# Kernel tuning notes

Measured on AMD Instinct MI355X. Metric: run time of the kernel, lower is better.

The kernel has to match this reference:

```python
import jax, jax.numpy as jnp
import numpy as np

B, N, H, F = 4, 512, 4096, 11008   # batch, seq, hidden, intermediate
L, R, RANK = 1, 16, 16             # layers stored, num adapters, lora rank
SCALE = 0.5                        # lora_scale


def setup_inputs() -> dict:
    key = jax.random.key(0)
    ks = jax.random.split(key, 12)
    nrm = lambda k, shape, fan: (jax.random.normal(k, shape, jnp.float32) * (fan ** -0.5))
    inp = {
        "x": jax.random.normal(ks[0], (B, N, H), jnp.float32),
        "W_gate": nrm(ks[1], (F, H), H),
        "W_up": nrm(ks[2], (F, H), H),
        "W_down": nrm(ks[3], (H, F), F),
        # LoRA tables: [num_layers, num_adapters, rank, in] and [num_layers, num_adapters, out, rank]
        "A_gate": nrm(ks[4], (L, R, RANK, H), H),
        "B_gate": nrm(ks[5], (L, R, F, RANK), RANK),
        "A_up": nrm(ks[6], (L, R, RANK, H), H),
        "B_up": nrm(ks[7], (L, R, F, RANK), RANK),
        "A_down": nrm(ks[8], (L, R, RANK, F), F),
        "B_down": nrm(ks[9], (L, R, H, RANK), RANK),
        "lora_indices": jax.random.randint(ks[10], (B,), 0, R),
        "layer_idx": 0,
    }
    return inp


def reference(x, W_gate, W_up, W_down, A_gate, B_gate, A_up, B_up,
              A_down, B_down, lora_indices, layer_idx):
    def lora_add(base, inp, A, B):
        # gather per-sequence adapter slices, then rank-r batched matmuls
        Ab = A[layer_idx][lora_indices]  # [B, r, in]
        Bb = B[layer_idx][lora_indices]  # [B, out, r]
        t = jnp.einsum('bri,bni->bnr', Ab, inp)        # down-project to rank
        return base + jnp.einsum('bor,bnr->bno', Bb, t) * SCALE

    gate = lora_add(jnp.einsum('bnh,fh->bnf', x, W_gate), x, A_gate, B_gate)
    up = lora_add(jnp.einsum('bnh,fh->bnf', x, W_up), x, A_up, B_up)
    act = jax.nn.silu(gate) * up                        # SwiGLU
    down = lora_add(jnp.einsum('bnf,hf->bnh', act, W_down), act, A_down, B_down)
    return down
```

## Files before the change

### kernel.cpp

```cpp
#include <hip/hip_runtime.h>
#include <hip/hip_bf16.h>

typedef __bf16 bf16x8 __attribute__((ext_vector_type(8)));
typedef float  f32x4  __attribute__((ext_vector_type(4)));
typedef unsigned short u16;

#define GLDS16(gsrc, ldst)                                                        \
  __builtin_amdgcn_global_load_lds(                                               \
      (const __attribute__((address_space(1))) unsigned int*)(gsrc),              \
      (__attribute__((address_space(3))) unsigned int*)(ldst), 16, 0, 0)

#define BAR() __builtin_amdgcn_s_barrier()
#define WAIT_LGKM0() asm volatile("s_waitcnt lgkmcnt(0)" ::: "memory")
#define WAIT_VM4() asm volatile("s_waitcnt vmcnt(4)" ::: "memory")

__device__ __forceinline__ u16 f2b(float f) {
  unsigned int u = __builtin_bit_cast(unsigned int, f);
  u = (u + 0x7fffu + ((u >> 16) & 1u)) >> 16;
  return (u16)u;
}
__device__ __forceinline__ float b2f(u16 b) {
  unsigned int u = ((unsigned int)b) << 16;
  return __builtin_bit_cast(float, u);
}

__global__ __launch_bounds__(256) void cvt3_kernel(
    const float4* __restrict__ xf,  ushort4* __restrict__ xb,
    const float4* __restrict__ wgf, ushort4* __restrict__ wgb,
    const float4* __restrict__ wuf, ushort4* __restrict__ wub) {
  const float4* in; ushort4* out; int i, stride, n4;
  if (blockIdx.x < 512) {
    in = xf; out = xb; n4 = 2097152;
    i = blockIdx.x * 256 + threadIdx.x; stride = 512 * 256;
  } else if (blockIdx.x < 2560) {
    in = wgf; out = wgb; n4 = 11272192;
    i = (blockIdx.x - 512) * 256 + threadIdx.x; stride = 2048 * 256;
  } else {
    in = wuf; out = wub; n4 = 11272192;
    i = (blockIdx.x - 2560) * 256 + threadIdx.x; stride = 2048 * 256;
  }
  for (; i < n4; i += stride) {
    float4 v = in[i];
    ushort4 o;
    o.x = f2b(v.x); o.y = f2b(v.y); o.z = f2b(v.z); o.w = f2b(v.w);
    out[i] = o;
  }
}

__global__ __launch_bounds__(256) void lora_t2(const u16* __restrict__ Xb, int K,
                                               const float* __restrict__ A1,
                                               const float* __restrict__ A2,
                                               const int* __restrict__ lidx,
                                               const int* __restrict__ layer,
                                               u16* __restrict__ t1,
                                               u16* __restrict__ t2) {
  __shared__ float red1[4][64][4];
  __shared__ float red2[4][64][4];
  const int lane = threadIdx.x & 63, wid = threadIdx.x >> 6;
  const int m0 = blockIdx.x * 16;
  const int li = lidx[m0 >> 9];
  const size_t abase = ((size_t)layer[0] * 16 + li) * 16 * (size_t)K;
  const int r = lane & 15, kg = lane >> 4;
  const int Kq = K >> 2, kb = wid * Kq;
  f32x4 acc1 = {0.f, 0.f, 0.f, 0.f}, acc2 = {0.f, 0.f, 0.f, 0.f};
  for (int k0 = kb; k0 < kb + Kq; k0 += 32) {
    bf16x8 a = *(const bf16x8*)&Xb[(size_t)(m0 + r) * K + k0 + kg * 8];
    const float* ap = A1 + abase + (size_t)r * K + k0 + kg * 8;
    float4 f0 = *(const float4*)ap;
    float4 f1 = *(const float4*)(ap + 4);
    bf16x8 b;
    b[0] = (__bf16)f0.x; b[1] = (__bf16)f0.y; b[2] = (__bf16)f0.z; b[3] = (__bf16)f0.w;
    b[4] = (__bf16)f1.x; b[5] = (__bf16)f1.y; b[6] = (__bf16)f1.z; b[7] = (__bf16)f1.w;
    acc1 = __builtin_amdgcn_mfma_f32_16x16x32_bf16(a, b, acc1, 0, 0, 0);
    if (A2) {
      const float* ap2 = A2 + abase + (size_t)r * K + k0 + kg * 8;
      float4 g0 = *(const float4*)ap2;
      float4 g1 = *(const float4*)(ap2 + 4);
      bf16x8 b2;
      b2[0] = (__bf16)g0.x; b2[1] = (__bf16)g0.y; b2[2] = (__bf16)g0.z; b2[3] = (__bf16)g0.w;
      b2[4] = (__bf16)g1.x; b2[5] = (__bf16)g1.y; b2[6] = (__bf16)g1.z; b2[7] = (__bf16)g1.w;
      acc2 = __builtin_amdgcn_mfma_f32_16x16x32_bf16(a, b2, acc2, 0, 0, 0);
    }
  }
#pragma unroll
  for (int j = 0; j < 4; ++j) {
    red1[wid][lane][j] = acc1[j];
    if (A2) red2[wid][lane][j] = acc2[j];
  }
  __syncthreads();
  if (wid == 0) {
#pragma unroll
    for (int j = 0; j < 4; ++j) {
      int m = m0 + kg * 4 + j;
      float v1 = red1[0][lane][j] + red1[1][lane][j] + red1[2][lane][j] + red1[3][lane][j];
      t1[(size_t)m * 16 + r] = f2b(0.5f * v1);
      if (A2) {
        float v2 = red2[0][lane][j] + red2[1][lane][j] + red2[2][lane][j] + red2[3][lane][j];
        t2[(size_t)m * 16 + r] = f2b(0.5f * v2);
      }
    }
  }
}

#define RD_A(dst, buf, mh) do {                                                \
    _Pragma("unroll")                                                          \
    for (int mf_ = 0; mf_ < 4; ++mf_)                                          \
      _Pragma("unroll")                                                        \
      for (int ks_ = 0; ks_ < 2; ++ks_) {                                      \
        int row_ = wm * 128 + (mh) * 64 + mf_ * 16 + lr;                       \
        int sl_ = (ks_ * 4 + kg) ^ rx;                                         \
        dst[mf_][ks_] = *(const bf16x8*)&sA[(buf) * 16384 + row_ * 64 + sl_ * 8]; \
      }                                                                        \
  } while (0)

#define RD_B(dst, buf, nh) do {                                                \
    _Pragma("unroll")                                                          \
    for (int nf_ = 0; nf_ < 2; ++nf_)                                          \
      _Pragma("unroll")                                                        \
      for (int ks_ = 0; ks_ < 2; ++ks_) {                                      \
        int row_ = wn * 64 + (nh) * 32 + nf_ * 16 + lr;                        \
        int sl_ = (ks_ * 4 + kg) ^ rx;                                         \
        dst[nf_][ks_] = *(const bf16x8*)&sB[(buf) * 16384 + row_ * 64 + sl_ * 8]; \
      }                                                                        \
  } while (0)

#define RD_BW(dst, SB, buf) do {                                               \
    _Pragma("unroll")                                                          \
    for (int nf_ = 0; nf_ < 2; ++nf_)                                          \
      _Pragma("unroll")                                                        \
      for (int ks_ = 0; ks_ < 2; ++ks_) {                                      \
        int row_ = wn * 32 + nf_ * 16 + lr;                                    \
        int sl_ = (ks_ * 4 + kg) ^ rx;                                         \
        dst[nf_][ks_] = *(const bf16x8*)&SB[(buf) * 8192 + row_ * 64 + sl_ * 8]; \
      }                                                                        \
  } while (0)

#define MMA_Q(AF, BF, mb, nb) do {                                             \
    __builtin_amdgcn_s_setprio(1);                                             \
    _Pragma("unroll")                                                          \
    for (int mf_ = 0; mf_ < 4; ++mf_)                                          \
      _Pragma("unroll")                                                        \
      for (int nf_ = 0; nf_ < 2; ++nf_)                                        \
        _Pragma("unroll")                                                      \
        for (int ks_ = 0; ks_ < 2; ++ks_)                                      \
          acc[(mb) + mf_][(nb) + nf_] = __builtin_amdgcn_mfma_f32_16x16x32_bf16( \
              AF[mf_][ks_], BF[nf_][ks_], acc[(mb) + mf_][(nb) + nf_], 0, 0, 0); \
    __builtin_amdgcn_s_setprio(0);                                             \
  } while (0)

#define MMA_F(AF, BF, ACC, mb) do {                                            \
    __builtin_amdgcn_s_setprio(1);                                             \
    _Pragma("unroll")                                                          \
    for (int mf_ = 0; mf_ < 4; ++mf_)                                          \
      _Pragma("unroll")                                                        \
      for (int nf_ = 0; nf_ < 2; ++nf_)                                        \
        _Pragma("unroll")                                                      \
        for (int ks_ = 0; ks_ < 2; ++ks_)                                      \
          ACC[(mb) + mf_][nf_] = __builtin_amdgcn_mfma_f32_16x16x32_bf16(      \
              AF[mf_][ks_], BF[nf_][ks_], ACC[(mb) + mf_][nf_], 0, 0, 0);      \
    __builtin_amdgcn_s_setprio(0);                                             \
  } while (0)

#define STAGE_F(buf, half, kt) do {                                            \
    const u16* gs_; u16* ld_;                                                  \
    if ((half) == 0)      { gs_ = Xb + (size_t)m0 * 4096 + (size_t)(kt) * 64;         ld_ = sA  + (buf) * 16384; }        \
    else if ((half) == 1) { gs_ = Xb + (size_t)(m0 + 128) * 4096 + (size_t)(kt) * 64; ld_ = sA  + (buf) * 16384 + 8192; } \
    else if ((half) == 2) { gs_ = Wg + (size_t)n0 * 4096 + (size_t)(kt) * 64;         ld_ = sBG + (buf) * 8192; }         \
    else                  { gs_ = Wu + (size_t)n0 * 4096 + (size_t)(kt) * 64;         ld_ = sBU + (buf) * 8192; }         \
    _Pragma("unroll")                                                          \
    for (int i_ = 0; i_ < 2; ++i_) {                                           \
      int ub_ = (wid << 6) + i_ * 512;                                         \
      int un_ = ub_ + lane;                                                    \
      int ur_ = un_ >> 3, us_ = (un_ & 7) ^ (ur_ & 7);                         \
      GLDS16(gs_ + (size_t)ur_ * 4096 + us_ * 8, ld_ + ub_ * 8);               \
    }                                                                          \
  } while (0)

__global__ __launch_bounds__(512, 2) void gemm_gup_fused(
    const u16* __restrict__ Xb, const u16* __restrict__ Wg, const u16* __restrict__ Wu,
    const u16* __restrict__ tg, const u16* __restrict__ tu,
    const float* __restrict__ Bg, const float* __restrict__ Bu,
    const int* __restrict__ lidx, const int* __restrict__ layer,
    u16* __restrict__ act,
    const float4* __restrict__ Wdf, ushort4* __restrict__ wdb3) {
  constexpr int F = 11008;
  const int b = blockIdx.x;
  if (b >= 704) {
    int i = (b - 704) * 512 + threadIdx.x;
    for (; i < 11272192; i += 256 * 512) {
      float4 v = Wdf[i];
      ushort4 o;
      o.x = f2b(v.x); o.y = f2b(v.y); o.z = f2b(v.z); o.w = f2b(v.w);
      wdb3[i] = o;
    }
    return;
  }
  const int xcd = b & 7, j = b >> 3;
  const int ny = xcd + 8 * (j >> 3);
  const int mx = j & 7;
  if (ny >= 86) return;
  extern __shared__ u16 smem[];
  u16* sA  = smem;
  u16* sBG = smem + 32768;
  u16* sBU = smem + 49152;
  const int tid = threadIdx.x, lane = tid & 63, wid = tid >> 6;
  const int lr = lane & 15, kg = lane >> 4, rx = lr & 7;
  const int wm = wid >> 2, wn = wid & 3;
  const int m0 = mx * 256;
  const int n0 = ny * 128;

  f32x4 accg[8][2] = {}, accu[8][2] = {};
  bf16x8 a0[4][2], a1[4][2], bg[2][2], bu[2][2];

  STAGE_F(0, 0, 0); STAGE_F(0, 1, 0); STAGE_F(0, 2, 0); STAGE_F(0, 3, 0);
  STAGE_F(1, 2, 1); STAGE_F(1, 3, 1);
  WAIT_VM4(); BAR();

#pragma unroll 1
  for (int u = 0; u < 32; ++u) {
    const int ktA = (2 * u + 1) & 63;
    const int kt0 = (2 * u + 2) & 63;
    const int kt1 = (2 * u + 3) & 63;
    RD_A(a0, 0, 0); RD_BW(bg, sBG, 0);
    STAGE_F(1, 0, ktA);
    BAR(); WAIT_LGKM0();
    MMA_F(a0, bg, accg, 0);
    BAR();
    RD_BW(bu, sBU, 0);
    STAGE_F(1, 1, ktA);
    BAR(); WAIT_LGKM0();
    MMA_F(a0, bu, accu, 0);
    BAR();
    RD_A(a1, 0, 1);
    STAGE_F(0, 2, kt0);
    BAR(); WAIT_LGKM0();
    MMA_F(a1, bu, accu, 4);
    BAR();
    STAGE_F(0, 3, kt0);
    BAR();
    MMA_F(a1, bg, accg, 4);
    WAIT_VM4();
    BAR();
    RD_A(a0, 1, 0); RD_BW(bg, sBG, 1);
    STAGE_F(0, 0, kt0); STAGE_F(0, 1, kt0);
    BAR(); WAIT_LGKM0();
    MMA_F(a0, bg, accg, 0);
    BAR();
    RD_BW(bu, sBU, 1);
    BAR(); WAIT_LGKM0();
    MMA_F(a0, bu, accu, 0);
    BAR();
    RD_A(a1, 1, 1);
    STAGE_F(1, 2, kt1);
    BAR(); WAIT_LGKM0();
    MMA_F(a1, bu, accu, 4);
    BAR();
    STAGE_F(1, 3, kt1);
    BAR();
    MMA_F(a1, bg, accg, 4);
    WAIT_VM4();
    BAR();
  }

  const int li = lidx[m0 >> 9];
  const size_t bbase = ((size_t)layer[0] * 16 + li) * (size_t)F * 16;
  bf16x8 la[8], lb[2];
  const bf16x8 zz = {};
#pragma unroll
  for (int mf = 0; mf < 8; ++mf) {
    int row = m0 + wm * 128 + mf * 16 + lr;
    la[mf] = (kg < 2) ? *(const bf16x8*)&tg[(size_t)row * 16 + kg * 8] : zz;
  }
#pragma unroll
  for (int nf = 0; nf < 2; ++nf) {
    int col = n0 + wn * 32 + nf * 16 + lr;
    if (kg < 2) {
      const float* bp = Bg + bbase + (size_t)col * 16 + kg * 8;
      float4 f0 = *(const float4*)bp;
      float4 f1 = *(const float4*)(bp + 4);
      bf16x8 v;
      v[0] = (__bf16)f0.x; v[1] = (__bf16)f0.y; v[2] = (__bf16)f0.z; v[3] = (__bf16)f0.w;
      v[4] = (__bf16)f1.x; v[5] = (__bf16)f1.y; v[6] = (__bf16)f1.z; v[7] = (__bf16)f1.w;
      lb[nf] = v;
    } else lb[nf] = zz;
  }
#pragma unroll
  for (int mf = 0; mf < 8; ++mf)
#pragma unroll
    for (int nf = 0; nf < 2; ++nf)
      accg[mf][nf] = __builtin_amdgcn_mfma_f32_16x16x32_bf16(la[mf], lb[nf], accg[mf][nf], 0, 0, 0);
#pragma unroll
  for (int mf = 0; mf < 8; ++mf) {
    int row = m0 + wm * 128 + mf * 16 + lr;
    la[mf] = (kg < 2) ? *(const bf16x8*)&tu[(size_t)row * 16 + kg * 8] : zz;
  }
#pragma unroll
  for (int nf = 0; nf < 2; ++nf) {
    int col = n0 + wn * 32 + nf * 16 + lr;
    if (kg < 2) {
      const float* bp = Bu + bbase + (size_t)col * 16 + kg * 8;
      float4 f0 = *(const float4*)bp;
      float4 f1 = *(const float4*)(bp + 4);
      bf16x8 v;
      v[0] = (__bf16)f0.x; v[1] = (__bf16)f0.y; v[2] = (__bf16)f0.z; v[3] = (__bf16)f0.w;
      v[4] = (__bf16)f1.x; v[5] = (__bf16)f1.y; v[6] = (__bf16)f1.z; v[7] = (__bf16)f1.w;
      lb[nf] = v;
    } else lb[nf] = zz;
  }
#pragma unroll
  for (int mf = 0; mf < 8; ++mf)
#pragma unroll
    for (int nf = 0; nf < 2; ++nf)
      accu[mf][nf] = __builtin_amdgcn_mfma_f32_16x16x32_bf16(la[mf], lb[nf], accu[mf][nf], 0, 0, 0);

#pragma unroll
  for (int mf = 0; mf < 8; ++mf)
#pragma unroll
    for (int nf = 0; nf < 2; ++nf)
#pragma unroll
      for (int j2 = 0; j2 < 4; ++j2) {
        int row = m0 + wm * 128 + mf * 16 + kg * 4 + j2;
        int col = n0 + wn * 32 + nf * 16 + lr;
        float g = accg[mf][nf][j2], uu = accu[mf][nf][j2];
        float s = g / (1.f + __expf(-g));
        act[(size_t)row * F + col] = f2b(s * uu);
      }
}

#define STAGE_D(buf, half, kt) do {                                           \
    int r0_ = ((half) & 1) * 128;                                             \
    const u16* gs_ = ((half) < 2)                                             \
        ? (Ab + (size_t)(m0 + r0_) * 11008 + (size_t)(kt) * 64)               \
        : (Wd + (size_t)(n0 + r0_) * 11008 + (size_t)(kt) * 64);              \
    u16* ld_ = (((half) < 2) ? sA : sB) + (buf) * 16384 + r0_ * 64;           \
    _Pragma("unroll")                                                         \
    for (int i_ = 0; i_ < 2; ++i_) {                                          \
      int ub_ = (wid << 6) + i_ * 512;                                        \
      int un_ = ub_ + lane;                                                   \
      int ur_ = un_ >> 3, us_ = (un_ & 7) ^ (ur_ & 7);                        \
      GLDS16(gs_ + (size_t)ur_ * 11008 + us_ * 8, ld_ + ub_ * 8);             \
    }                                                                         \
  } while (0)

#define KT(t) (kbase + ((t) >= 86 ? (t) - 86 : (t)))

__global__ __launch_bounds__(512, 2) void gemm_down8(
    const u16* __restrict__ Ab, const u16* __restrict__ Wd,
    const u16* __restrict__ td, const float* __restrict__ Bd,
    const int* __restrict__ lidx, const int* __restrict__ layer,
    float* __restrict__ P0, float* __restrict__ P1) {
  constexpr int H = 4096;
  extern __shared__ u16 smem[];
  u16* sA = smem;
  u16* sB = smem + 32768;
  const int tid = threadIdx.x, lane = tid & 63, wid = tid >> 6;
  const int lr = lane & 15, kg = lane >> 4, rx = lr & 7;
  const int wm = wid >> 2, wn = wid & 3;
  const int m0 = blockIdx.x * 256, n0 = blockIdx.y * 256;
  const int kbase = blockIdx.z * 86;
  float* P = blockIdx.z ? P1 : P0;

  f32x4 acc[8][4] = {};
  bf16x8 a0[4][2], a1[4][2], b0[2][2], b1[2][2];

  STAGE_D(0, 0, KT(0)); STAGE_D(0, 1, KT(0)); STAGE_D(0, 2, KT(0)); STAGE_D(0, 3, KT(0));
  STAGE_D(1, 2, KT(1)); STAGE_D(1, 3, KT(1));
  WAIT_VM4(); BAR();

#pragma unroll 1
  for (int u = 0; u < 43; ++u) {
    const int ktA = KT(2 * u + 1);
    const int kt0 = KT(2 * u + 2);
    const int kt1 = KT(2 * u + 3);
    RD_A(a0, 0, 0); RD_B(b0, 0, 0);
    STAGE_D(1, 0, ktA);
    BAR(); WAIT_LGKM0();
    MMA_Q(a0, b0, 0, 0);
    BAR();
    RD_B(b1, 0, 1);
    STAGE_D(1, 1, ktA);
    BAR(); WAIT_LGKM0();
    MMA_Q(a0, b1, 0, 2);
    BAR();
    RD_A(a1, 0, 1);
    STAGE_D(0, 2, kt0);
    BAR(); WAIT_LGKM0();
    MMA_Q(a1, b1, 4, 2);
    BAR();
    STAGE_D(0, 3, kt0);
    BAR();
    MMA_Q(a1, b0, 4, 0);
    WAIT_VM4();
    BAR();
    RD_A(a0, 1, 0); RD_B(b0, 1, 0);
    STAGE_D(0, 0, kt0);
    BAR(); WAIT_LGKM0();
    MMA_Q(a0, b0, 0, 0);
    BAR();
    RD_B(b1, 1, 1);
    STAGE_D(0, 1, kt0);
    BAR(); WAIT_LGKM0();
    MMA_Q(a0, b1, 0, 2);
    BAR();
    RD_A(a1, 1, 1);
    STAGE_D(1, 2, kt1);
    BAR(); WAIT_LGKM0();
    MMA_Q(a1, b1, 4, 2);
    BAR();
    STAGE_D(1, 3, kt1);
    BAR();
    MMA_Q(a1, b0, 4, 0);
    WAIT_VM4();
    BAR();
  }

  if (blockIdx.z == 0) {
    const int li = lidx[m0 >> 9];
    const size_t bbase = ((size_t)layer[0] * 16 + li) * (size_t)H * 16;
    bf16x8 la[8], lb[4];
    const bf16x8 zz = {};
#pragma unroll
    for (int mf = 0; mf < 8; ++mf) {
      int row = m0 + wm * 128 + mf * 16 + lr;
      la[mf] = (kg < 2) ? *(const bf16x8*)&td[(size_t)row * 16 + kg * 8] : zz;
    }
#pragma unroll
    for (int nf = 0; nf < 4; ++nf) {
      int col = n0 + wn * 64 + nf * 16 + lr;
      if (kg < 2) {
        const float* bp = Bd + bbase + (size_t)col * 16 + kg * 8;
        float4 f0 = *(const float4*)bp;
        float4 f1 = *(const float4*)(bp + 4);
        bf16x8 v;
        v[0] = (__bf16)f0.x; v[1] = (__bf16)f0.y; v[2] = (__bf16)f0.z; v[3] = (__bf16)f0.w;
        v[4] = (__bf16)f1.x; v[5] = (__bf16)f1.y; v[6] = (__bf16)f1.z; v[7] = (__bf16)f1.w;
        lb[nf] = v;
      } else lb[nf] = zz;
    }
#pragma unroll
    for (int mf = 0; mf < 8; ++mf)
#pragma unroll
      for (int nf = 0; nf < 4; ++nf)
        acc[mf][nf] = __builtin_amdgcn_mfma_f32_16x16x32_bf16(la[mf], lb[nf], acc[mf][nf], 0, 0, 0);
  }

#pragma unroll
  for (int mf = 0; mf < 8; ++mf)
#pragma unroll
    for (int nf = 0; nf < 4; ++nf)
#pragma unroll
      for (int j = 0; j < 4; ++j) {
        int row = m0 + wm * 128 + mf * 16 + kg * 4 + j;
        int col = n0 + wn * 64 + nf * 16 + lr;
        P[(size_t)row * H + col] = acc[mf][nf][j];
      }
}

__global__ __launch_bounds__(256) void combine_down(
    const float4* __restrict__ P0, const float4* __restrict__ P1,
    float4* __restrict__ out) {
  int gid = blockIdx.x * 256 + threadIdx.x;
  float4 p0 = P0[gid], p1 = P1[gid];
  out[gid] = make_float4(p0.x + p1.x, p0.y + p1.y, p0.z + p1.z, p0.w + p1.w);
}

extern "C" void kernel_launch(void* const* d_in, const int* in_sizes, int n_in,
                              void* d_out, int out_size, void* d_ws, size_t ws_size,
                              hipStream_t stream) {
  const float* x  = (const float*)d_in[0];
  const float* Wg = (const float*)d_in[1];
  const float* Wu = (const float*)d_in[2];
  const float* Wd = (const float*)d_in[3];
  const float* Ag = (const float*)d_in[4];
  const float* Bg = (const float*)d_in[5];
  const float* Au = (const float*)d_in[6];
  const float* Bu = (const float*)d_in[7];
  const float* Ad = (const float*)d_in[8];
  const float* Bd = (const float*)d_in[9];
  const int* lidx = (const int*)d_in[10];
  const int* lay  = (const int*)d_in[11];
  float* out = (float*)d_out;

  char* ws = (char*)d_ws;
  u16*  xb   = (u16*)(ws + 0);
  u16*  wgb  = (u16*)(ws + 16777216);
  u16*  wub  = (u16*)(ws + 106954752);
  u16*  gbuf = (u16*)(ws + 197132288);
  u16*  tg   = (u16*)(ws + 287309824);
  u16*  tu   = (u16*)(ws + 287375360);
  u16*  td   = (u16*)(ws + 287440896);
  u16*  wdb3 = (u16*)(ws + 287506432);
  float* P0  = (float*)(ws + 242221056);
  float* P1  = (float*)wub;

  hipFuncSetAttribute(reinterpret_cast<const void*>(gemm_gup_fused),
                      hipFuncAttributeMaxDynamicSharedMemorySize, 131072);
  hipFuncSetAttribute(reinterpret_cast<const void*>(gemm_down8),
                      hipFuncAttributeMaxDynamicSharedMemorySize, 131072);

  cvt3_kernel<<<4608, 256, 0, stream>>>((const float4*)x,  (ushort4*)xb,
                                        (const float4*)Wg, (ushort4*)wgb,
                                        (const float4*)Wu, (ushort4*)wub);

  lora_t2<<<128, 256, 0, stream>>>(xb, 4096, Ag, Au, lidx, lay, tg, tu);

  gemm_gup_fused<<<dim3(960), 512, 131072, stream>>>(
      xb, wgb, wub, tg, tu, Bg, Bu, lidx, lay, gbuf,
      (const float4*)Wd, (ushort4*)wdb3);

  lora_t2<<<128, 256, 0, stream>>>(gbuf, 11008, Ad, nullptr, lidx, lay, td, nullptr);

  gemm_down8<<<dim3(8, 16, 2), 512, 131072, stream>>>(gbuf, wdb3, td, Bd, lidx, lay,
                                                      P0, P1);

  combine_down<<<8192, 256, 0, stream>>>((const float4*)P0, (const float4*)P1,
                                         (float4*)out);
}
```

Measured before the change: 732.8 us.

## Replace split-K down GEMM and combine pass with 256x128 tiles writing output directly

The down-projection GEMM previously used 256x256 tiles with a 2-way K split, writing two fp32 partial buffers that a separate combine kernel summed. The new kernel uses 256x128 tiles over the full K range, 256 blocks mapped by an XCD-aware index, and writes the final output directly with the LoRA term added. This removes the partial-buffer writes and reads and one kernel launch. In exchange, each block reads more A data per unit of work, runs a longer K loop, and uses a different staging schedule with less shared memory.

```diff
diff --git a/kernel.cpp b/kernel.cpp
--- a/kernel.cpp
+++ b/kernel.cpp
@@ -12,6 +12,7 @@
 
 #define BAR() __builtin_amdgcn_s_barrier()
 #define WAIT_LGKM0() asm volatile("s_waitcnt lgkmcnt(0)" ::: "memory")
+#define WAIT_VM0() asm volatile("s_waitcnt vmcnt(0)" ::: "memory")
 #define WAIT_VM4() asm volatile("s_waitcnt vmcnt(4)" ::: "memory")
 
 __device__ __forceinline__ u16 f2b(float f) {
@@ -113,17 +114,6 @@
       }                                                                        \
   } while (0)
 
-#define RD_B(dst, buf, nh) do {                                                \
-    _Pragma("unroll")                                                          \
-    for (int nf_ = 0; nf_ < 2; ++nf_)                                          \
-      _Pragma("unroll")                                                        \
-      for (int ks_ = 0; ks_ < 2; ++ks_) {                                      \
-        int row_ = wn * 64 + (nh) * 32 + nf_ * 16 + lr;                        \
-        int sl_ = (ks_ * 4 + kg) ^ rx;                                         \
-        dst[nf_][ks_] = *(const bf16x8*)&sB[(buf) * 16384 + row_ * 64 + sl_ * 8]; \
-      }                                                                        \
-  } while (0)
-
 #define RD_BW(dst, SB, buf) do {                                               \
     _Pragma("unroll")                                                          \
     for (int nf_ = 0; nf_ < 2; ++nf_)                                          \
@@ -133,19 +123,6 @@
         int sl_ = (ks_ * 4 + kg) ^ rx;                                         \
         dst[nf_][ks_] = *(const bf16x8*)&SB[(buf) * 8192 + row_ * 64 + sl_ * 8]; \
       }                                                                        \
-  } while (0)
-
-#define MMA_Q(AF, BF, mb, nb) do {                                             \
-    __builtin_amdgcn_s_setprio(1);                                             \
-    _Pragma("unroll")                                                          \
-    for (int mf_ = 0; mf_ < 4; ++mf_)                                          \
-      _Pragma("unroll")                                                        \
-      for (int nf_ = 0; nf_ < 2; ++nf_)                                        \
-        _Pragma("unroll")                                                      \
-        for (int ks_ = 0; ks_ < 2; ++ks_)                                      \
-          acc[(mb) + mf_][(nb) + nf_] = __builtin_amdgcn_mfma_f32_16x16x32_bf16( \
-              AF[mf_][ks_], BF[nf_][ks_], acc[(mb) + mf_][(nb) + nf_], 0, 0, 0); \
-    __builtin_amdgcn_s_setprio(0);                                             \
   } while (0)
 
 #define MMA_F(AF, BF, ACC, mb) do {                                            \
@@ -327,141 +304,125 @@
       }
 }
 
-#define STAGE_D(buf, half, kt) do {                                           \
-    int r0_ = ((half) & 1) * 128;                                             \
-    const u16* gs_ = ((half) < 2)                                             \
-        ? (Ab + (size_t)(m0 + r0_) * 11008 + (size_t)(kt) * 64)               \
-        : (Wd + (size_t)(n0 + r0_) * 11008 + (size_t)(kt) * 64);              \
-    u16* ld_ = (((half) < 2) ? sA : sB) + (buf) * 16384 + r0_ * 64;           \
-    _Pragma("unroll")                                                         \
-    for (int i_ = 0; i_ < 2; ++i_) {                                          \
-      int ub_ = (wid << 6) + i_ * 512;                                        \
-      int un_ = ub_ + lane;                                                   \
-      int ur_ = un_ >> 3, us_ = (un_ & 7) ^ (ur_ & 7);                        \
-      GLDS16(gs_ + (size_t)ur_ * 11008 + us_ * 8, ld_ + ub_ * 8);             \
-    }                                                                         \
-  } while (0)
-
-#define KT(t) (kbase + ((t) >= 86 ? (t) - 86 : (t)))
-
-__global__ __launch_bounds__(512, 2) void gemm_down8(
+#define STAGE_NA(buf, half, kt) do {                                           \
+    const u16* gs_ = Ab + (size_t)(m0 + (half) * 128) * 11008 + (size_t)(kt) * 64; \
+    u16* ld_ = sA + (buf) * 16384 + (half) * 8192;                             \
+    _Pragma("unroll")                                                          \
+    for (int i_ = 0; i_ < 2; ++i_) {                                           \
+      int ub_ = (wid << 6) + i_ * 512;                                         \
+      int un_ = ub_ + lane;                                                    \
+      int ur_ = un_ >> 3, us_ = (un_ & 7) ^ (ur_ & 7);                         \
+      GLDS16(gs_ + (size_t)ur_ * 11008 + us_ * 8, ld_ + ub_ * 8);              \
+    }                                                                          \
+  } while (0)
+
+#define STAGE_NB(buf, kt) do {                                                 \
+    const u16* gs_ = Wd + (size_t)n0 * 11008 + (size_t)(kt) * 64;              \
+    u16* ld_ = sB + (buf) * 8192;                                              \
+    _Pragma("unroll")                                                          \
+    for (int i_ = 0; i_ < 2; ++i_) {                                           \
+      int ub_ = (wid << 6) + i_ * 512;                                         \
+      int un_ = ub_ + lane;                                                    \
+      int ur_ = un_ >> 3, us_ = (un_ & 7) ^ (ur_ & 7);                         \
+      GLDS16(gs_ + (size_t)ur_ * 11008 + us_ * 8, ld_ + ub_ * 8);              \
+    }                                                                          \
+  } while (0)
+
+#define KTW(t) ((t) >= 172 ? (t) - 172 : (t))
+
+__global__ __launch_bounds__(512, 2) void gemm_down_ns(
     const u16* __restrict__ Ab, const u16* __restrict__ Wd,
     const u16* __restrict__ td, const float* __restrict__ Bd,
     const int* __restrict__ lidx, const int* __restrict__ layer,
-    float* __restrict__ P0, float* __restrict__ P1) {
+    float* __restrict__ out) {
   constexpr int H = 4096;
   extern __shared__ u16 smem[];
   u16* sA = smem;
   u16* sB = smem + 32768;
+  const int b = blockIdx.x;
+  const int xcd = b & 7, j = b >> 3;
+  const int ny = xcd + 8 * (j >> 3);
+  const int mx = j & 7;
   const int tid = threadIdx.x, lane = tid & 63, wid = tid >> 6;
   const int lr = lane & 15, kg = lane >> 4, rx = lr & 7;
   const int wm = wid >> 2, wn = wid & 3;
-  const int m0 = blockIdx.x * 256, n0 = blockIdx.y * 256;
-  const int kbase = blockIdx.z * 86;
-  float* P = blockIdx.z ? P1 : P0;
-
-  f32x4 acc[8][4] = {};
-  bf16x8 a0[4][2], a1[4][2], b0[2][2], b1[2][2];
-
-  STAGE_D(0, 0, KT(0)); STAGE_D(0, 1, KT(0)); STAGE_D(0, 2, KT(0)); STAGE_D(0, 3, KT(0));
-  STAGE_D(1, 2, KT(1)); STAGE_D(1, 3, KT(1));
-  WAIT_VM4(); BAR();
+  const int m0 = mx * 256;
+  const int n0 = ny * 128;
+
+  f32x4 acc[8][2] = {};
+  bf16x8 a0[4][2], a1[4][2], bw[2][2];
+
+  STAGE_NA(0, 0, 0); STAGE_NA(0, 1, 0); STAGE_NB(0, 0);
+  STAGE_NA(1, 0, 1); STAGE_NB(1, 1);
+  WAIT_VM0(); BAR();
 
 #pragma unroll 1
-  for (int u = 0; u < 43; ++u) {
-    const int ktA = KT(2 * u + 1);
-    const int kt0 = KT(2 * u + 2);
-    const int kt1 = KT(2 * u + 3);
-    RD_A(a0, 0, 0); RD_B(b0, 0, 0);
-    STAGE_D(1, 0, ktA);
-    BAR(); WAIT_LGKM0();
-    MMA_Q(a0, b0, 0, 0);
-    BAR();
-    RD_B(b1, 0, 1);
-    STAGE_D(1, 1, ktA);
-    BAR(); WAIT_LGKM0();
-    MMA_Q(a0, b1, 0, 2);
+  for (int u = 0; u < 86; ++u) {
+    const int ktA = KTW(2 * u + 1);
+    const int kt0 = KTW(2 * u + 2);
+    const int kt1 = KTW(2 * u + 3);
+    RD_A(a0, 0, 0); RD_BW(bw, sB, 0);
+    STAGE_NA(1, 1, ktA);
+    BAR(); WAIT_LGKM0();
+    MMA_F(a0, bw, acc, 0);
     BAR();
     RD_A(a1, 0, 1);
-    STAGE_D(0, 2, kt0);
-    BAR(); WAIT_LGKM0();
-    MMA_Q(a1, b1, 4, 2);
-    BAR();
-    STAGE_D(0, 3, kt0);
-    BAR();
-    MMA_Q(a1, b0, 4, 0);
+    STAGE_NA(0, 0, kt0); STAGE_NB(0, kt0);
+    BAR(); WAIT_LGKM0();
+    MMA_F(a1, bw, acc, 4);
     WAIT_VM4();
     BAR();
-    RD_A(a0, 1, 0); RD_B(b0, 1, 0);
-    STAGE_D(0, 0, kt0);
-    BAR(); WAIT_LGKM0();
-    MMA_Q(a0, b0, 0, 0);
-    BAR();
-    RD_B(b1, 1, 1);
-    STAGE_D(0, 1, kt0);
-    BAR(); WAIT_LGKM0();
-    MMA_Q(a0, b1, 0, 2);
+    RD_A(a0, 1, 0); RD_BW(bw, sB, 1);
+    STAGE_NA(0, 1, kt0);
+    BAR(); WAIT_LGKM0();
+    MMA_F(a0, bw, acc, 0);
     BAR();
     RD_A(a1, 1, 1);
-    STAGE_D(1, 2, kt1);
-    BAR(); WAIT_LGKM0();
-    MMA_Q(a1, b1, 4, 2);
-    BAR();
-    STAGE_D(1, 3, kt1);
-    BAR();
-    MMA_Q(a1, b0, 4, 0);
+    STAGE_NA(1, 0, kt1); STAGE_NB(1, kt1);
+    BAR(); WAIT_LGKM0();
+    MMA_F(a1, bw, acc, 4);
     WAIT_VM4();
     BAR();
   }
 
-  if (blockIdx.z == 0) {
-    const int li = lidx[m0 >> 9];
-    const size_t bbase = ((size_t)layer[0] * 16 + li) * (size_t)H * 16;
-    bf16x8 la[8], lb[4];
-    const bf16x8 zz = {};
-#pragma unroll
-    for (int mf = 0; mf < 8; ++mf) {
-      int row = m0 + wm * 128 + mf * 16 + lr;
-      la[mf] = (kg < 2) ? *(const bf16x8*)&td[(size_t)row * 16 + kg * 8] : zz;
-    }
-#pragma unroll
-    for (int nf = 0; nf < 4; ++nf) {
-      int col = n0 + wn * 64 + nf * 16 + lr;
-      if (kg < 2) {
-        const float* bp = Bd + bbase + (size_t)col * 16 + kg * 8;
-        float4 f0 = *(const float4*)bp;
-        float4 f1 = *(const float4*)(bp + 4);
-        bf16x8 v;
-        v[0] = (__bf16)f0.x; v[1] = (__bf16)f0.y; v[2] = (__bf16)f0.z; v[3] = (__bf16)f0.w;
-        v[4] = (__bf16)f1.x; v[5] = (__bf16)f1.y; v[6] = (__bf16)f1.z; v[7] = (__bf16)f1.w;
-        lb[nf] = v;
-      } else lb[nf] = zz;
-    }
-#pragma unroll
-    for (int mf = 0; mf < 8; ++mf)
-#pragma unroll
-      for (int nf = 0; nf < 4; ++nf)
-        acc[mf][nf] = __builtin_amdgcn_mfma_f32_16x16x32_bf16(la[mf], lb[nf], acc[mf][nf], 0, 0, 0);
-  }
-
+  const int li = lidx[m0 >> 9];
+  const size_t bbase = ((size_t)layer[0] * 16 + li) * (size_t)H * 16;
+  bf16x8 la[8], lb[2];
+  const bf16x8 zz = {};
+#pragma unroll
+  for (int mf = 0; mf < 8; ++mf) {
+    int row = m0 + wm * 128 + mf * 16 + lr;
+    la[mf] = (kg < 2) ? *(const bf16x8*)&td[(size_t)row * 16 + kg * 8] : zz;
+  }
+#pragma unroll
+  for (int nf = 0; nf < 2; ++nf) {
+    int col = n0 + wn * 32 + nf * 16 + lr;
+    if (kg < 2) {
+      const float* bp = Bd + bbase + (size_t)col * 16 + kg * 8;
+      float4 f0 = *(const float4*)bp;
+      float4 f1 = *(const float4*)(bp + 4);
+      bf16x8 v;
+      v[0] = (__bf16)f0.x; v[1] = (__bf16)f0.y; v[2] = (__bf16)f0.z; v[3] = (__bf16)f0.w;
+      v[4] = (__bf16)f1.x; v[5] = (__bf16)f1.y; v[6] = (__bf16)f1.z; v[7] = (__bf16)f1.w;
+      lb[nf] = v;
+    } else lb[nf] = zz;
+  }
 #pragma unroll
   for (int mf = 0; mf < 8; ++mf)
 #pragma unroll
-    for (int nf = 0; nf < 4; ++nf)
-#pragma unroll
-      for (int j = 0; j < 4; ++j) {
-        int row = m0 + wm * 128 + mf * 16 + kg * 4 + j;
-        int col = n0 + wn * 64 + nf * 16 + lr;
-        P[(size_t)row * H + col] = acc[mf][nf][j];
+    for (int nf = 0; nf < 2; ++nf)
+      acc[mf][nf] = __builtin_amdgcn_mfma_f32_16x16x32_bf16(la[mf], lb[nf], acc[mf][nf], 0, 0, 0);
+
+#pragma unroll
+  for (int mf = 0; mf < 8; ++mf)
+#pragma unroll
+    for (int nf = 0; nf < 2; ++nf)
+#pragma unroll
+      for (int j2 = 0; j2 < 4; ++j2) {
+        int row = m0 + wm * 128 + mf * 16 + kg * 4 + j2;
+        int col = n0 + wn * 32 + nf * 16 + lr;
+        out[(size_t)row * H + col] = acc[mf][nf][j2];
       }
-}
-
-__global__ __launch_bounds__(256) void combine_down(
-    const float4* __restrict__ P0, const float4* __restrict__ P1,
-    float4* __restrict__ out) {
-  int gid = blockIdx.x * 256 + threadIdx.x;
-  float4 p0 = P0[gid], p1 = P1[gid];
-  out[gid] = make_float4(p0.x + p1.x, p0.y + p1.y, p0.z + p1.z, p0.w + p1.w);
 }
 
 extern "C" void kernel_launch(void* const* d_in, const int* in_sizes, int n_in,
@@ -490,13 +451,11 @@
   u16*  tu   = (u16*)(ws + 287375360);
   u16*  td   = (u16*)(ws + 287440896);
   u16*  wdb3 = (u16*)(ws + 287506432);
-  float* P0  = (float*)(ws + 242221056);
-  float* P1  = (float*)wub;
 
   hipFuncSetAttribute(reinterpret_cast<const void*>(gemm_gup_fused),
                       hipFuncAttributeMaxDynamicSharedMemorySize, 131072);
-  hipFuncSetAttribute(reinterpret_cast<const void*>(gemm_down8),
-                      hipFuncAttributeMaxDynamicSharedMemorySize, 131072);
+  hipFuncSetAttribute(reinterpret_cast<const void*>(gemm_down_ns),
+                      hipFuncAttributeMaxDynamicSharedMemorySize, 98304);
 
   cvt3_kernel<<<4608, 256, 0, stream>>>((const float4*)x,  (ushort4*)xb,
                                         (const float4*)Wg, (ushort4*)wgb,
@@ -510,9 +469,5 @@
 
   lora_t2<<<128, 256, 0, stream>>>(gbuf, 11008, Ad, nullptr, lidx, lay, td, nullptr);
 
-  gemm_down8<<<dim3(8, 16, 2), 512, 131072, stream>>>(gbuf, wdb3, td, Bd, lidx, lay,
-                                                      P0, P1);
-
-  combine_down<<<8192, 256, 0, stream>>>((const float4*)P0, (const float4*)P1,
-                                         (float4*)out);
-}
+  gemm_down_ns<<<dim3(256), 512, 98304, stream>>>(gbuf, wdb3, td, Bd, lidx, lay, out);
+}
```

Result: no change. 723.9 us, median of 2 (-1.2%).
